# Optimization experiments

Measured on AMD Instinct MI355X. Metric: run time of the kernel, lower is better.

Reference implementation:

```python
import jax, jax.numpy as jnp
import numpy as np

VOCAB = 32000
EMBED = 512
NUM_CLASS = 5
LEAVES = 8192
N_NODES = 2 * LEAVES - 1


def _build_tree(n_leaves):
    """Balanced binary tree over n_leaves leaves, nodes listed in post-order
    (children always appear before their parent), matching the recursive
    traversal order of the original torch module."""
    is_leaf, word, left, right = [], [], [], []

    def rec(lo, hi):
        if hi - lo == 1:
            is_leaf.append(1)
            word.append((lo * 2654435761) % VOCAB)
            left.append(0)
            right.append(0)
        else:
            mid = (lo + hi) // 2
            l = rec(lo, mid)
            r = rec(mid, hi)
            is_leaf.append(0)
            word.append(0)
            left.append(l)
            right.append(r)
        return len(is_leaf) - 1

    rec(0, n_leaves)
    return (np.asarray(is_leaf, np.int32), np.asarray(word, np.int32),
            np.asarray(left, np.int32), np.asarray(right, np.int32))


def setup_inputs() -> dict:
    key = jax.random.key(0)
    k1, k2, k3, k4, k5 = jax.random.split(key, 5)
    is_leaf, word, left, right = _build_tree(LEAVES)
    scale = 0.05
    return {
        "is_leaf": jnp.asarray(is_leaf),
        "word": jnp.asarray(word),
        "left": jnp.asarray(left),
        "right": jnp.asarray(right),
        "emb": jax.random.normal(k1, (VOCAB, EMBED), jnp.float32) * scale,
        "W": jax.random.normal(k2, (EMBED, 2 * EMBED), jnp.float32) * scale,
        "bW": jax.random.normal(k3, (EMBED,), jnp.float32) * scale,
        "P": jax.random.normal(k4, (NUM_CLASS, EMBED), jnp.float32) * scale,
        "bP": jax.random.normal(k5, (NUM_CLASS,), jnp.float32) * scale,
    }


def reference(is_leaf, word, left, right, emb, W, bW, P, bP):
    n = is_leaf.shape[0]

    def step(H, xs):
        idx, lf, wd, li, ri = xs
        # internal node: relu(W @ [h_left; h_right] + b)
        pair = jnp.concatenate([H[li], H[ri]])          # [2D]
        internal = pair @ W.T + bW                       # [D]
        leaf = emb[wd]                                   # [D]
        h = jax.nn.relu(jnp.where(lf == 1, leaf, internal))
        return H.at[idx].set(h), None

    H0 = jnp.zeros((n, EMBED), emb.dtype)
    xs = (jnp.arange(n, dtype=jnp.int32), is_leaf, word, left, right)
    H, _ = jax.lax.scan(step, H0, xs)
    # per-node class logits, rows in traversal (post-)order: [N, num_class]
    return H @ P.T + bP
```

## Files before the change

### kernel.cpp

```cpp
#include <hip/hip_runtime.h>


#define EMBED 512
#define K2    1024
#define WOFF  (EMBED * K2)

typedef _Float16 half8 __attribute__((ext_vector_type(8)));
typedef float    floatx4 __attribute__((ext_vector_type(4)));

__device__ __forceinline__ float relu_f(float x) { return fmaxf(x, 0.0f); }

#define GLDS16(gp, lp)                                                        \
    __builtin_amdgcn_global_load_lds(                                         \
        (const __attribute__((address_space(1))) void*)(gp),                  \
        (__attribute__((address_space(3))) void*)(lp), 16, 0, 0)

#define MFMA16(a, b, c) __builtin_amdgcn_mfma_f32_16x16x32_f16(a, b, c, 0, 0, 0)

__global__ __launch_bounds__(256)
void packleaf(const float* __restrict__ W, const float* __restrict__ emb,
              const int* __restrict__ word,
              _Float16* __restrict__ Whp,
              _Float16* __restrict__ Hh, _Float16* __restrict__ Hl,
              int nLeaves)
{
    int tid = threadIdx.x;
    int wave = tid >> 6, lane = tid & 63;

    {
        int t = blockIdx.x * 256 + tid;
        int n = t >> 7, kc = t & 127;
        const float* src = W + (size_t)n * K2 + kc * 8;
        int s = kc >> 2, quad = kc & 3;
        int ln = (quad << 4) | (n & 15);
        size_t off = (size_t)(n >> 4) * 16384 + (size_t)s * 512 + (size_t)ln * 8;
        half8 hi, lo;
#pragma unroll
        for (int j = 0; j < 8; ++j) {
            float w = src[j];
            _Float16 h16 = (_Float16)w;
            hi[j] = h16;
            lo[j] = (_Float16)(w - (float)h16);
        }
        *(half8*)(Whp + off) = hi;
        *(half8*)(Whp + WOFF + off) = lo;
    }
    {
#pragma unroll
        for (int i = 0; i < 8; ++i) {
            int m = blockIdx.x * 32 + wave * 8 + i;
            if (m < nLeaves) {
                int wd = word[2 * m - __popc(m)];
                const float4* src = (const float4*)(emb + (size_t)wd * EMBED) + lane * 2;
                float4 a = src[0], b = src[1];
                float v[8] = {a.x, a.y, a.z, a.w, b.x, b.y, b.z, b.w};
                half8 hi, lo;
#pragma unroll
                for (int j = 0; j < 8; ++j) {
                    float x = relu_f(v[j]);
                    _Float16 h16 = (_Float16)x;
                    hi[j] = h16;
                    lo[j] = (_Float16)(x - (float)h16);
                }
                *(half8*)(Hh + (size_t)m * EMBED + lane * 8) = hi;
                *(half8*)(Hl + (size_t)m * EMBED + lane * 8) = lo;
            }
        }
    }
}

__global__ __launch_bounds__(256)
void gemm_lvl(const _Float16* __restrict__ Ap,
              const _Float16* __restrict__ Wp,
              const float* __restrict__ bW,
              _Float16* __restrict__ Cp,
              int hoff)
{
    __shared__ _Float16 As[16384];
    __shared__ float Red[4096];

    int tid = threadIdx.x;
    int wave = tid >> 6, lane = tid & 63;
    int q = lane >> 4, r = lane & 15;
    int slice = wave >> 1, nh = wave & 1;
    int bm0 = blockIdx.x * 64, bn0 = blockIdx.y * 64;

    const _Float16* Asrc = Ap + (size_t)(nh ? hoff : 0)
                         + (size_t)(bm0 + r) * 1024 + slice * 512 + q * 8;

    floatx4 acc[4][2];
#pragma unroll
    for (int t = 0; t < 4; ++t)
#pragma unroll
        for (int u = 0; u < 2; ++u) acc[t][u] = (floatx4){0.f, 0.f, 0.f, 0.f};

    for (int kc = 0; kc < 8; ++kc) {
#pragma unroll
        for (int t = 0; t < 4; ++t)
#pragma unroll
            for (int s2 = 0; s2 < 2; ++s2) {
                const _Float16* gp = Asrc + t * (16 * 1024) + kc * 64 + s2 * 32;
                GLDS16(gp, &As[(slice * 16 + t * 4 + s2 * 2 + nh) * 512]);
            }
        __syncthreads();

#pragma unroll
        for (int s2 = 0; s2 < 2; ++s2) {
            half8 bh[2], bl[2];
#pragma unroll
            for (int u = 0; u < 2; ++u) {
                const _Float16* pb = Wp + (size_t)(blockIdx.y * 4 + nh * 2 + u) * 16384
                                   + (size_t)(slice * 16 + kc * 2 + s2) * 512 + lane * 8;
                bh[u] = *(const half8*)pb;
                bl[u] = *(const half8*)(pb + WOFF);
            }
#pragma unroll
            for (int t = 0; t < 4; ++t) {
                half8 ah = *(const half8*)&As[(slice * 16 + t * 4 + s2 * 2 + 0) * 512 + lane * 8];
                half8 al = *(const half8*)&As[(slice * 16 + t * 4 + s2 * 2 + 1) * 512 + lane * 8];
#pragma unroll
                for (int u = 0; u < 2; ++u) {
                    acc[t][u] = MFMA16(ah, bh[u], acc[t][u]);
                    acc[t][u] = MFMA16(ah, bl[u], acc[t][u]);
                    acc[t][u] = MFMA16(al, bh[u], acc[t][u]);
                }
            }
        }
        __syncthreads();
    }

    if (slice == 1) {
#pragma unroll
        for (int t = 0; t < 4; ++t)
#pragma unroll
            for (int u = 0; u < 2; ++u)
#pragma unroll
                for (int reg = 0; reg < 4; ++reg)
                    Red[(t * 16 + q * 4 + reg) * 64 + nh * 32 + u * 16 + r]
                        = acc[t][u][reg];
    }
    __syncthreads();
    if (slice == 0) {
#pragma unroll
        for (int t = 0; t < 4; ++t)
#pragma unroll
            for (int u = 0; u < 2; ++u) {
                int col = bn0 + nh * 32 + u * 16 + r;
                float bw = bW[col];
#pragma unroll
                for (int reg = 0; reg < 4; ++reg) {
                    int ml = t * 16 + q * 4 + reg;
                    float v = acc[t][u][reg]
                            + Red[ml * 64 + nh * 32 + u * 16 + r];
                    float x = relu_f(v + bw);
                    _Float16 hi = (_Float16)x;
                    size_t o = (size_t)(bm0 + ml) * EMBED + col;
                    Cp[o] = hi;
                    Cp[o + hoff] = (_Float16)(x - (float)hi);
                }
            }
    }
}

__global__ __launch_bounds__(256)
void gemm_splitk32(const _Float16* __restrict__ Ap, const _Float16* __restrict__ Wp,
                   const float* __restrict__ bW,
                   _Float16* __restrict__ Cp, int hoff)
{
    __shared__ float red[4096];

    int tid = threadIdx.x;
    int wave = tid >> 6, lane = tid & 63;
    int q = lane >> 4, r = lane & 15;
    int m0 = blockIdx.x * 32, n0 = blockIdx.y * 32;

    const _Float16 *pAh[2], *pAl[2];
#pragma unroll
    for (int mi = 0; mi < 2; ++mi) {
        int m = m0 + mi * 16 + r;
        int prow = 2 * m + (wave >> 1);
        int kb = (wave & 1) * 256;
        pAh[mi] = Ap + (size_t)prow * EMBED + kb + q * 8;
        pAl[mi] = pAh[mi] + hoff;
    }
    const _Float16* pB[2];
#pragma unroll
    for (int u = 0; u < 2; ++u)
        pB[u] = Wp + (size_t)(blockIdx.y * 2 + u) * 16384
              + (size_t)(wave * 8) * 512 + lane * 8;

    floatx4 acc[2][2];
#pragma unroll
    for (int mi = 0; mi < 2; ++mi)
#pragma unroll
        for (int u = 0; u < 2; ++u) acc[mi][u] = (floatx4){0.f, 0.f, 0.f, 0.f};

#pragma unroll
    for (int s = 0; s < 8; ++s) {
        half8 ah[2], al[2], bh[2], bl[2];
#pragma unroll
        for (int mi = 0; mi < 2; ++mi) {
            ah[mi] = *(const half8*)(pAh[mi] + s * 32);
            al[mi] = *(const half8*)(pAl[mi] + s * 32);
        }
#pragma unroll
        for (int u = 0; u < 2; ++u) {
            bh[u] = *(const half8*)(pB[u] + s * 512);
            bl[u] = *(const half8*)(pB[u] + s * 512 + WOFF);
        }
#pragma unroll
        for (int mi = 0; mi < 2; ++mi)
#pragma unroll
            for (int u = 0; u < 2; ++u) {
                acc[mi][u] = MFMA16(ah[mi], bh[u], acc[mi][u]);
                acc[mi][u] = MFMA16(ah[mi], bl[u], acc[mi][u]);
                acc[mi][u] = MFMA16(al[mi], bh[u], acc[mi][u]);
            }
    }

#pragma unroll
    for (int mi = 0; mi < 2; ++mi)
#pragma unroll
        for (int u = 0; u < 2; ++u)
#pragma unroll
            for (int reg = 0; reg < 4; ++reg)
                red[wave * 1024 + (mi * 16 + q * 4 + reg) * 32 + u * 16 + r]
                    = acc[mi][u][reg];
    __syncthreads();

    int row = tid >> 3, c4 = (tid & 7) * 4;
    _Float16 hi4[4], lo4[4];
#pragma unroll
    for (int j = 0; j < 4; ++j) {
        int c = row * 32 + c4 + j;
        float v = red[c] + red[1024 + c] + red[2048 + c] + red[3072 + c];
        float x = relu_f(v + bW[n0 + c4 + j]);
        _Float16 hi = (_Float16)x;
        hi4[j] = hi;
        lo4[j] = (_Float16)(x - (float)hi);
    }
    size_t o = (size_t)(m0 + row) * EMBED + n0 + c4;
#pragma unroll
    for (int j = 0; j < 4; ++j) { Cp[o + j] = hi4[j]; Cp[o + hoff + j] = lo4[j]; }
}

__global__ __launch_bounds__(256)
void gemm_splitk(const _Float16* __restrict__ Ap, const _Float16* __restrict__ Wp,
                 const float* __restrict__ bW,
                 _Float16* __restrict__ Cp, int hoff, int M)
{
    __shared__ float red[1024];

    int tid = threadIdx.x;
    int wave = tid >> 6, lane = tid & 63;
    int q = lane >> 4, r = lane & 15;
    int mt = blockIdx.x, u = blockIdx.y;

    int m = mt * 16 + r;
    if (m >= M) m = M - 1;
    int prow = 2 * m + (wave >> 1);
    int kb = (wave & 1) * 256;
    const _Float16* pAh = Ap + (size_t)prow * EMBED + kb + q * 8;
    const _Float16* pAl = pAh + hoff;
    const _Float16* pB  = Wp + (size_t)u * 16384 + (size_t)(wave * 8) * 512 + lane * 8;

    floatx4 acc = (floatx4){0.f, 0.f, 0.f, 0.f};
#pragma unroll
    for (int s = 0; s < 8; ++s) {
        half8 ah = *(const half8*)(pAh + s * 32);
        half8 al = *(const half8*)(pAl + s * 32);
        half8 bh = *(const half8*)(pB + s * 512);
        half8 bl = *(const half8*)(pB + s * 512 + WOFF);
        acc = MFMA16(ah, bh, acc);
        acc = MFMA16(ah, bl, acc);
        acc = MFMA16(al, bh, acc);
    }
#pragma unroll
    for (int reg = 0; reg < 4; ++reg)
        red[wave * 256 + (q * 4 + reg) * 16 + r] = acc[reg];
    __syncthreads();

    int row = tid >> 4, col = tid & 15;
    float v = red[row * 16 + col] + red[256 + row * 16 + col]
            + red[512 + row * 16 + col] + red[768 + row * 16 + col];
    int mm = mt * 16 + row;
    if (mm < M) {
        int colg = u * 16 + col;
        float x = relu_f(v + bW[colg]);
        _Float16 hi = (_Float16)x;
        size_t o = (size_t)mm * EMBED + colg;
        Cp[o] = hi;
        Cp[o + hoff] = (_Float16)(x - (float)hi);
    }
}

__global__ __launch_bounds__(256)
void out_kernel(const _Float16* __restrict__ Hh, const _Float16* __restrict__ Hl,
                const float* __restrict__ P, const float* __restrict__ bP,
                float* __restrict__ out, int nNodes)
{
    int t = blockIdx.x * 256 + threadIdx.x;
    int j = t >> 6, lane = t & 63;
    if (j >= nNodes) return;
    int v = nNodes - j;
    int h = 13 - (31 - __clz(v));
    int m = j - ((nNodes + 1) - (1 << (13 - h + 1)));
    int node = ((m + 1) << (h + 1)) - 2 - __popc(m);

    half8 hv = *(const half8*)(Hh + (size_t)j * EMBED + lane * 8);
    half8 lv = *(const half8*)(Hl + (size_t)j * EMBED + lane * 8);
    float hx[8];
#pragma unroll
    for (int k = 0; k < 8; ++k) hx[k] = (float)hv[k] + (float)lv[k];
    float s[5];
#pragma unroll
    for (int c = 0; c < 5; ++c) {
        const float* p = P + c * EMBED + lane * 8;
        float4 p0 = *(const float4*)p;
        float4 p1 = *(const float4*)(p + 4);
        s[c] = hx[0] * p0.x + hx[1] * p0.y + hx[2] * p0.z + hx[3] * p0.w
             + hx[4] * p1.x + hx[5] * p1.y + hx[6] * p1.z + hx[7] * p1.w;
    }
#pragma unroll
    for (int o = 32; o > 0; o >>= 1)
#pragma unroll
        for (int c = 0; c < 5; ++c)
            s[c] += __shfl_down(s[c], o, 64);
    if (lane == 0) {
#pragma unroll
        for (int c = 0; c < 5; ++c)
            out[(size_t)node * 5 + c] = s[c] + bP[c];
    }
}

extern "C" void kernel_launch(void* const* d_in, const int* in_sizes, int n_in,
                              void* d_out, int out_size, void* d_ws, size_t ws_size,
                              hipStream_t stream)
{
    const int*   word = (const int*)d_in[1];
    const float* emb  = (const float*)d_in[4];
    const float* W    = (const float*)d_in[5];
    const float* bW   = (const float*)d_in[6];
    const float* P    = (const float*)d_in[7];
    const float* bP   = (const float*)d_in[8];
    float* out = (float*)d_out;

    int nNodes  = in_sizes[0];
    int nLeaves = (nNodes + 1) / 2;
    int nRows   = nNodes + 1;

    int hoff = nRows * EMBED;
    _Float16* Hh  = (_Float16*)d_ws;
    _Float16* Hl  = Hh + hoff;
    _Float16* Whp = Hl + hoff;

    auto roff = [&](int h) { return nRows - (1 << (14 - h)); };

    packleaf<<<dim3(256), dim3(256), 0, stream>>>(
        W, emb, word, Whp, Hh, Hl, nLeaves);

    for (int h = 1; h <= 2; ++h) {
        int M = 1 << (13 - h);
        gemm_lvl<<<dim3(M / 64, 8), dim3(256), 0, stream>>>(
            Hh + (size_t)roff(h - 1) * EMBED, Whp, bW,
            Hh + (size_t)roff(h) * EMBED, hoff);
    }
    for (int h = 3; h <= 4; ++h) {
        int M = 1 << (13 - h);
        gemm_splitk32<<<dim3(M / 32, 16), dim3(256), 0, stream>>>(
            Hh + (size_t)roff(h - 1) * EMBED, Whp, bW,
            Hh + (size_t)roff(h) * EMBED, hoff);
    }
    for (int h = 5; h <= 13; ++h) {
        int M = 1 << (13 - h);
        gemm_splitk<<<dim3((M + 15) / 16, 32), dim3(256), 0, stream>>>(
            Hh + (size_t)roff(h - 1) * EMBED, Whp, bW,
            Hh + (size_t)roff(h) * EMBED, hoff, M);
    }
    out_kernel<<<dim3((nNodes * 64 + 255) / 256), dim3(256), 0, stream>>>(
        Hh, Hl, P, bP, out, nNodes);
}
```

Measured before the change: 235.5 us.

## Replace split-K level GEMM with double-buffered full-K 128-row tiles

The first two tree-level GEMMs now use a templated kernel with 128-row tiles where each wave owns 32 rows across the full K=1024. This removes the split-K LDS reduction and the extra barrier. A/Alow tiles are double-buffered in LDS through async global-to-LDS loads with explicit vmcnt waits, so loads overlap with MFMA work. The N-tile width is templated per level (128 or 64 columns) to keep grid sizes at 128 blocks. The larger LDS footprint and fewer blocks may reduce occupancy.

Measured after the change: 290.3 us. 23.2% more time.

```diff
diff --git a/kernel.cpp b/kernel.cpp
--- a/kernel.cpp
+++ b/kernel.cpp
@@ -69,97 +69,101 @@
     }
 }
 
-__global__ __launch_bounds__(256)
-void gemm_lvl(const _Float16* __restrict__ Ap,
+template <int BNF>
+__global__ __launch_bounds__(256, 2)
+void gemm_big(const _Float16* __restrict__ Ap,
               const _Float16* __restrict__ Wp,
               const float* __restrict__ bW,
               _Float16* __restrict__ Cp,
               int hoff)
 {
-    __shared__ _Float16 As[16384];
-    __shared__ float Red[4096];
+    __shared__ _Float16 As[32768];
 
     int tid = threadIdx.x;
-    int wave = tid >> 6, lane = tid & 63;
+    int w = tid >> 6, lane = tid & 63;
     int q = lane >> 4, r = lane & 15;
-    int slice = wave >> 1, nh = wave & 1;
-    int bm0 = blockIdx.x * 64, bn0 = blockIdx.y * 64;
-
-    const _Float16* Asrc = Ap + (size_t)(nh ? hoff : 0)
-                         + (size_t)(bm0 + r) * 1024 + slice * 512 + q * 8;
-
-    floatx4 acc[4][2];
-#pragma unroll
-    for (int t = 0; t < 4; ++t)
-#pragma unroll
-        for (int u = 0; u < 2; ++u) acc[t][u] = (floatx4){0.f, 0.f, 0.f, 0.f};
-
-    for (int kc = 0; kc < 8; ++kc) {
-#pragma unroll
-        for (int t = 0; t < 4; ++t)
-#pragma unroll
-            for (int s2 = 0; s2 < 2; ++s2) {
-                const _Float16* gp = Asrc + t * (16 * 1024) + kc * 64 + s2 * 32;
-                GLDS16(gp, &As[(slice * 16 + t * 4 + s2 * 2 + nh) * 512]);
-            }
-        __syncthreads();
+    int bm0 = blockIdx.x * 128;
+    int bn0 = blockIdx.y * (BNF * 16);
+
+    const _Float16* Asrc = Ap + (size_t)(bm0 + w * 32 + r) * 1024 + q * 8;
+
+    floatx4 acc[2][BNF];
+#pragma unroll
+    for (int t2 = 0; t2 < 2; ++t2)
+#pragma unroll
+        for (int u = 0; u < BNF; ++u) acc[t2][u] = (floatx4){0.f, 0.f, 0.f, 0.f};
+
+#pragma unroll
+    for (int t2 = 0; t2 < 2; ++t2)
+#pragma unroll
+        for (int s2 = 0; s2 < 2; ++s2)
+#pragma unroll
+            for (int hl = 0; hl < 2; ++hl) {
+                const _Float16* gp = Asrc + (size_t)hl * hoff
+                                   + t2 * (16 * 1024) + s2 * 32;
+                GLDS16(gp, &As[(((w * 2 + t2) * 2 + s2) * 2 + hl) * 512]);
+            }
+
+    for (int kc = 0; kc < 16; ++kc) {
+        int buf = kc & 1;
+        if (kc < 15) {
+#pragma unroll
+            for (int t2 = 0; t2 < 2; ++t2)
+#pragma unroll
+                for (int s2 = 0; s2 < 2; ++s2)
+#pragma unroll
+                    for (int hl = 0; hl < 2; ++hl) {
+                        const _Float16* gp = Asrc + (size_t)hl * hoff
+                                           + t2 * (16 * 1024) + (kc + 1) * 64 + s2 * 32;
+                        GLDS16(gp, &As[((buf ^ 1) * 32
+                                        + ((w * 2 + t2) * 2 + s2) * 2 + hl) * 512]);
+                    }
+            asm volatile("s_waitcnt vmcnt(8)" ::: "memory");
+        } else {
+            asm volatile("s_waitcnt vmcnt(0)" ::: "memory");
+        }
 
 #pragma unroll
         for (int s2 = 0; s2 < 2; ++s2) {
-            half8 bh[2], bl[2];
-#pragma unroll
-            for (int u = 0; u < 2; ++u) {
-                const _Float16* pb = Wp + (size_t)(blockIdx.y * 4 + nh * 2 + u) * 16384
-                                   + (size_t)(slice * 16 + kc * 2 + s2) * 512 + lane * 8;
-                bh[u] = *(const half8*)pb;
-                bl[u] = *(const half8*)(pb + WOFF);
-            }
-#pragma unroll
-            for (int t = 0; t < 4; ++t) {
-                half8 ah = *(const half8*)&As[(slice * 16 + t * 4 + s2 * 2 + 0) * 512 + lane * 8];
-                half8 al = *(const half8*)&As[(slice * 16 + t * 4 + s2 * 2 + 1) * 512 + lane * 8];
-#pragma unroll
-                for (int u = 0; u < 2; ++u) {
-                    acc[t][u] = MFMA16(ah, bh[u], acc[t][u]);
-                    acc[t][u] = MFMA16(ah, bl[u], acc[t][u]);
-                    acc[t][u] = MFMA16(al, bh[u], acc[t][u]);
+            half8 ah[2], al[2];
+#pragma unroll
+            for (int t2 = 0; t2 < 2; ++t2) {
+                int slot = buf * 32 + ((w * 2 + t2) * 2 + s2) * 2;
+                ah[t2] = *(const half8*)&As[slot * 512 + lane * 8];
+                al[t2] = *(const half8*)&As[(slot + 1) * 512 + lane * 8];
+            }
+#pragma unroll
+            for (int u = 0; u < BNF; ++u) {
+                const _Float16* pb = Wp + (size_t)(blockIdx.y * BNF + u) * 16384
+                                   + (size_t)(kc * 2 + s2) * 512 + lane * 8;
+                half8 bh = *(const half8*)pb;
+                half8 bl = *(const half8*)(pb + WOFF);
+#pragma unroll
+                for (int t2 = 0; t2 < 2; ++t2) {
+                    acc[t2][u] = MFMA16(ah[t2], bh, acc[t2][u]);
+                    acc[t2][u] = MFMA16(ah[t2], bl, acc[t2][u]);
+                    acc[t2][u] = MFMA16(al[t2], bh, acc[t2][u]);
                 }
             }
         }
-        __syncthreads();
-    }
-
-    if (slice == 1) {
-#pragma unroll
-        for (int t = 0; t < 4; ++t)
-#pragma unroll
-            for (int u = 0; u < 2; ++u)
-#pragma unroll
-                for (int reg = 0; reg < 4; ++reg)
-                    Red[(t * 16 + q * 4 + reg) * 64 + nh * 32 + u * 16 + r]
-                        = acc[t][u][reg];
-    }
-    __syncthreads();
-    if (slice == 0) {
-#pragma unroll
-        for (int t = 0; t < 4; ++t)
-#pragma unroll
-            for (int u = 0; u < 2; ++u) {
-                int col = bn0 + nh * 32 + u * 16 + r;
-                float bw = bW[col];
-#pragma unroll
-                for (int reg = 0; reg < 4; ++reg) {
-                    int ml = t * 16 + q * 4 + reg;
-                    float v = acc[t][u][reg]
-                            + Red[ml * 64 + nh * 32 + u * 16 + r];
-                    float x = relu_f(v + bw);
-                    _Float16 hi = (_Float16)x;
-                    size_t o = (size_t)(bm0 + ml) * EMBED + col;
-                    Cp[o] = hi;
-                    Cp[o + hoff] = (_Float16)(x - (float)hi);
-                }
-            }
-    }
+    }
+
+#pragma unroll
+    for (int t2 = 0; t2 < 2; ++t2)
+#pragma unroll
+        for (int u = 0; u < BNF; ++u) {
+            int col = bn0 + u * 16 + r;
+            float bw = bW[col];
+#pragma unroll
+            for (int reg = 0; reg < 4; ++reg) {
+                int row = bm0 + (w * 2 + t2) * 16 + q * 4 + reg;
+                float x = relu_f(acc[t2][u][reg] + bw);
+                _Float16 hi = (_Float16)x;
+                size_t o = (size_t)row * EMBED + col;
+                Cp[o] = hi;
+                Cp[o + hoff] = (_Float16)(x - (float)hi);
+            }
+        }
 }
 
 __global__ __launch_bounds__(256)
@@ -359,12 +363,13 @@
     packleaf<<<dim3(256), dim3(256), 0, stream>>>(
         W, emb, word, Whp, Hh, Hl, nLeaves);
 
-    for (int h = 1; h <= 2; ++h) {
-        int M = 1 << (13 - h);
-        gemm_lvl<<<dim3(M / 64, 8), dim3(256), 0, stream>>>(
-            Hh + (size_t)roff(h - 1) * EMBED, Whp, bW,
-            Hh + (size_t)roff(h) * EMBED, hoff);
-    }
+    gemm_big<8><<<dim3(32, 4), dim3(256), 0, stream>>>(
+        Hh + (size_t)roff(0) * EMBED, Whp, bW,
+        Hh + (size_t)roff(1) * EMBED, hoff);
+    gemm_big<4><<<dim3(16, 8), dim3(256), 0, stream>>>(
+        Hh + (size_t)roff(1) * EMBED, Whp, bW,
+        Hh + (size_t)roff(2) * EMBED, hoff);
+
     for (int h = 3; h <= 4; ++h) {
         int M = 1 << (13 - h);
         gemm_splitk32<<<dim3(M / 32, 16), dim3(256), 0, stream>>>(
```

## Fuse class-logit projection into leaf and level GEMM epilogues via atomics

Applied to the files above, without the earlier changes.

Removes the separate output kernel that reread all hidden states to compute per-node logits. Each leaf-packing block and each level GEMM epilogue now computes partial dot products of its fresh activations with P and atomically accumulates them into outputs pre-initialised with bP by a new init kernel. This avoids a full pass over the hi/lo hidden buffers. In exchange it adds an extra launch, extra syncs and shared-memory traffic in gemm_lvl, float atomics whose summation order is nondeterministic, and logits computed from fp32 values instead of the hi+lo reconstruction.

New measurement: 274.7 us. 16.6% more time.

```diff
diff --git a/kernel.cpp b/kernel.cpp
--- a/kernel.cpp
+++ b/kernel.cpp
@@ -16,13 +16,21 @@
         (__attribute__((address_space(3))) void*)(lp), 16, 0, 0)
 
 #define MFMA16(a, b, c) __builtin_amdgcn_mfma_f32_16x16x32_f16(a, b, c, 0, 0, 0)
+
+__global__ __launch_bounds__(256)
+void init_out(const float* __restrict__ bP, float* __restrict__ out, int n5)
+{
+    int i = blockIdx.x * 256 + threadIdx.x;
+    if (i < n5) out[i] = bP[i - (i / 5) * 5];
+}
 
 __global__ __launch_bounds__(256)
 void packleaf(const float* __restrict__ W, const float* __restrict__ emb,
               const int* __restrict__ word,
               _Float16* __restrict__ Whp,
               _Float16* __restrict__ Hh, _Float16* __restrict__ Hl,
-              int nLeaves)
+              const float* __restrict__ P, const float* __restrict__ bP,
+              float* __restrict__ out, int nLeaves)
 {
     int tid = threadIdx.x;
     int wave = tid >> 6, lane = tid & 63;
@@ -50,20 +58,42 @@
         for (int i = 0; i < 8; ++i) {
             int m = blockIdx.x * 32 + wave * 8 + i;
             if (m < nLeaves) {
-                int wd = word[2 * m - __popc(m)];
+                int node = 2 * m - __popc(m);
+                int wd = word[node];
                 const float4* src = (const float4*)(emb + (size_t)wd * EMBED) + lane * 2;
                 float4 a = src[0], b = src[1];
                 float v[8] = {a.x, a.y, a.z, a.w, b.x, b.y, b.z, b.w};
+                float xs[8];
                 half8 hi, lo;
 #pragma unroll
                 for (int j = 0; j < 8; ++j) {
                     float x = relu_f(v[j]);
+                    xs[j] = x;
                     _Float16 h16 = (_Float16)x;
                     hi[j] = h16;
                     lo[j] = (_Float16)(x - (float)h16);
                 }
                 *(half8*)(Hh + (size_t)m * EMBED + lane * 8) = hi;
                 *(half8*)(Hl + (size_t)m * EMBED + lane * 8) = lo;
+                float s[5];
+#pragma unroll
+                for (int c = 0; c < 5; ++c) {
+                    const float* p = P + c * EMBED + lane * 8;
+                    float4 p0 = *(const float4*)p;
+                    float4 p1 = *(const float4*)(p + 4);
+                    s[c] = xs[0] * p0.x + xs[1] * p0.y + xs[2] * p0.z + xs[3] * p0.w
+                         + xs[4] * p1.x + xs[5] * p1.y + xs[6] * p1.z + xs[7] * p1.w;
+                }
+#pragma unroll
+                for (int o = 32; o > 0; o >>= 1)
+#pragma unroll
+                    for (int c = 0; c < 5; ++c)
+                        s[c] += __shfl_down(s[c], o, 64);
+                if (lane == 0) {
+#pragma unroll
+                    for (int c = 0; c < 5; ++c)
+                        out[(size_t)node * 5 + c] = s[c] + bP[c];
+                }
             }
         }
     }
@@ -74,7 +104,8 @@
               const _Float16* __restrict__ Wp,
               const float* __restrict__ bW,
               _Float16* __restrict__ Cp,
-              int hoff)
+              int hoff,
+              const float* __restrict__ P, float* __restrict__ out, int lvl)
 {
     __shared__ _Float16 As[16384];
     __shared__ float Red[4096];
@@ -129,6 +160,7 @@
         __syncthreads();
     }
 
+    float xv[4][2][4];
     if (slice == 1) {
 #pragma unroll
         for (int t = 0; t < 4; ++t)
@@ -153,6 +185,7 @@
                     float v = acc[t][u][reg]
                             + Red[ml * 64 + nh * 32 + u * 16 + r];
                     float x = relu_f(v + bw);
+                    xv[t][u][reg] = x;
                     _Float16 hi = (_Float16)x;
                     size_t o = (size_t)(bm0 + ml) * EMBED + col;
                     Cp[o] = hi;
@@ -160,12 +193,50 @@
                 }
             }
     }
+    __syncthreads();
+    if (slice == 0) {
+#pragma unroll
+        for (int t = 0; t < 4; ++t)
+#pragma unroll
+            for (int u = 0; u < 2; ++u)
+#pragma unroll
+            for (int reg = 0; reg < 4; ++reg)
+                Red[(t * 16 + q * 4 + reg) * 64 + nh * 32 + u * 16 + r]
+                    = xv[t][u][reg];
+    }
+    __syncthreads();
+    {
+        int prow = tid >> 2, seg = tid & 3;
+        float s[5] = {0.f, 0.f, 0.f, 0.f, 0.f};
+#pragma unroll
+        for (int j4 = 0; j4 < 4; ++j4) {
+            floatx4 xq = *(const floatx4*)&Red[prow * 64 + seg * 16 + j4 * 4];
+#pragma unroll
+            for (int c = 0; c < 5; ++c) {
+                float4 pq = *(const float4*)&P[c * EMBED + bn0 + seg * 16 + j4 * 4];
+                s[c] += xq[0] * pq.x + xq[1] * pq.y + xq[2] * pq.z + xq[3] * pq.w;
+            }
+        }
+#pragma unroll
+        for (int c = 0; c < 5; ++c) {
+            s[c] += __shfl_xor(s[c], 1, 64);
+            s[c] += __shfl_xor(s[c], 2, 64);
+        }
+        if (seg == 0) {
+            int mrow = bm0 + prow;
+            int node = ((mrow + 1) << (lvl + 1)) - 2 - __popc(mrow);
+#pragma unroll
+            for (int c = 0; c < 5; ++c)
+                atomicAdd(&out[(size_t)node * 5 + c], s[c]);
+        }
+    }
 }
 
 __global__ __launch_bounds__(256)
 void gemm_splitk32(const _Float16* __restrict__ Ap, const _Float16* __restrict__ Wp,
                    const float* __restrict__ bW,
-                   _Float16* __restrict__ Cp, int hoff)
+                   _Float16* __restrict__ Cp, int hoff,
+                   const float* __restrict__ P, float* __restrict__ out, int lvl)
 {
     __shared__ float red[4096];
 
@@ -229,12 +300,14 @@
     __syncthreads();
 
     int row = tid >> 3, c4 = (tid & 7) * 4;
+    float xf[4];
     _Float16 hi4[4], lo4[4];
 #pragma unroll
     for (int j = 0; j < 4; ++j) {
         int c = row * 32 + c4 + j;
         float v = red[c] + red[1024 + c] + red[2048 + c] + red[3072 + c];
         float x = relu_f(v + bW[n0 + c4 + j]);
+        xf[j] = x;
         _Float16 hi = (_Float16)x;
         hi4[j] = hi;
         lo4[j] = (_Float16)(x - (float)hi);
@@ -242,12 +315,32 @@
     size_t o = (size_t)(m0 + row) * EMBED + n0 + c4;
 #pragma unroll
     for (int j = 0; j < 4; ++j) { Cp[o + j] = hi4[j]; Cp[o + hoff + j] = lo4[j]; }
+
+    {
+        float s[5];
+#pragma unroll
+        for (int c = 0; c < 5; ++c) {
+            float4 pq = *(const float4*)&P[c * EMBED + n0 + c4];
+            s[c] = xf[0] * pq.x + xf[1] * pq.y + xf[2] * pq.z + xf[3] * pq.w;
+            s[c] += __shfl_xor(s[c], 1, 64);
+            s[c] += __shfl_xor(s[c], 2, 64);
+            s[c] += __shfl_xor(s[c], 4, 64);
+        }
+        if ((tid & 7) == 0) {
+            int mrow = m0 + row;
+            int node = ((mrow + 1) << (lvl + 1)) - 2 - __popc(mrow);
+#pragma unroll
+            for (int c = 0; c < 5; ++c)
+                atomicAdd(&out[(size_t)node * 5 + c], s[c]);
+        }
+    }
 }
 
 __global__ __launch_bounds__(256)
 void gemm_splitk(const _Float16* __restrict__ Ap, const _Float16* __restrict__ Wp,
                  const float* __restrict__ bW,
-                 _Float16* __restrict__ Cp, int hoff, int M)
+                 _Float16* __restrict__ Cp, int hoff, int M,
+                 const float* __restrict__ P, float* __restrict__ out, int lvl)
 {
     __shared__ float red[1024];
 
@@ -284,52 +377,30 @@
     float v = red[row * 16 + col] + red[256 + row * 16 + col]
             + red[512 + row * 16 + col] + red[768 + row * 16 + col];
     int mm = mt * 16 + row;
+    int colg = u * 16 + col;
+    float x = relu_f(v + bW[colg]);
     if (mm < M) {
-        int colg = u * 16 + col;
-        float x = relu_f(v + bW[colg]);
         _Float16 hi = (_Float16)x;
         size_t o = (size_t)mm * EMBED + colg;
         Cp[o] = hi;
         Cp[o + hoff] = (_Float16)(x - (float)hi);
     }
-}
-
-__global__ __launch_bounds__(256)
-void out_kernel(const _Float16* __restrict__ Hh, const _Float16* __restrict__ Hl,
-                const float* __restrict__ P, const float* __restrict__ bP,
-                float* __restrict__ out, int nNodes)
-{
-    int t = blockIdx.x * 256 + threadIdx.x;
-    int j = t >> 6, lane = t & 63;
-    if (j >= nNodes) return;
-    int v = nNodes - j;
-    int h = 13 - (31 - __clz(v));
-    int m = j - ((nNodes + 1) - (1 << (13 - h + 1)));
-    int node = ((m + 1) << (h + 1)) - 2 - __popc(m);
-
-    half8 hv = *(const half8*)(Hh + (size_t)j * EMBED + lane * 8);
-    half8 lv = *(const half8*)(Hl + (size_t)j * EMBED + lane * 8);
-    float hx[8];
-#pragma unroll
-    for (int k = 0; k < 8; ++k) hx[k] = (float)hv[k] + (float)lv[k];
-    float s[5];
-#pragma unroll
-    for (int c = 0; c < 5; ++c) {
-        const float* p = P + c * EMBED + lane * 8;
-        float4 p0 = *(const float4*)p;
-        float4 p1 = *(const float4*)(p + 4);
-        s[c] = hx[0] * p0.x + hx[1] * p0.y + hx[2] * p0.z + hx[3] * p0.w
-             + hx[4] * p1.x + hx[5] * p1.y + hx[6] * p1.z + hx[7] * p1.w;
-    }
-#pragma unroll
-    for (int o = 32; o > 0; o >>= 1)
-#pragma unroll
-        for (int c = 0; c < 5; ++c)
-            s[c] += __shfl_down(s[c], o, 64);
-    if (lane == 0) {
-#pragma unroll
-        for (int c = 0; c < 5; ++c)
-            out[(size_t)node * 5 + c] = s[c] + bP[c];
+    {
+        float s[5];
+#pragma unroll
+        for (int c = 0; c < 5; ++c) {
+            s[c] = x * P[c * EMBED + colg];
+            s[c] += __shfl_xor(s[c], 1, 64);
+            s[c] += __shfl_xor(s[c], 2, 64);
+            s[c] += __shfl_xor(s[c], 4, 64);
+            s[c] += __shfl_xor(s[c], 8, 64);
+        }
+        if (col == 0 && mm < M) {
+            int node = ((mm + 1) << (lvl + 1)) - 2 - __popc(mm);
+#pragma unroll
+            for (int c = 0; c < 5; ++c)
+                atomicAdd(&out[(size_t)node * 5 + c], s[c]);
+        }
     }
 }
 
@@ -356,27 +427,28 @@
 
     auto roff = [&](int h) { return nRows - (1 << (14 - h)); };
 
+    int n5 = nNodes * 5;
+    init_out<<<dim3((n5 + 255) / 256), dim3(256), 0, stream>>>(bP, out, n5);
+
     packleaf<<<dim3(256), dim3(256), 0, stream>>>(
-        W, emb, word, Whp, Hh, Hl, nLeaves);
+        W, emb, word, Whp, Hh, Hl, P, bP, out, nLeaves);
 
     for (int h = 1; h <= 2; ++h) {
         int M = 1 << (13 - h);
         gemm_lvl<<<dim3(M / 64, 8), dim3(256), 0, stream>>>(
             Hh + (size_t)roff(h - 1) * EMBED, Whp, bW,
-            Hh + (size_t)roff(h) * EMBED, hoff);
+            Hh + (size_t)roff(h) * EMBED, hoff, P, out, h);
     }
     for (int h = 3; h <= 4; ++h) {
         int M = 1 << (13 - h);
         gemm_splitk32<<<dim3(M / 32, 16), dim3(256), 0, stream>>>(
             Hh + (size_t)roff(h - 1) * EMBED, Whp, bW,
-            Hh + (size_t)roff(h) * EMBED, hoff);
+            Hh + (size_t)roff(h) * EMBED, hoff, P, out, h);
     }
     for (int h = 5; h <= 13; ++h) {
         int M = 1 << (13 - h);
         gemm_splitk<<<dim3((M + 15) / 16, 32), dim3(256), 0, stream>>>(
             Hh + (size_t)roff(h - 1) * EMBED, Whp, bW,
-            Hh + (size_t)roff(h) * EMBED, hoff, M);
-    }
-    out_kernel<<<dim3((nNodes * 64 + 255) / 256), dim3(256), 0, stream>>>(
-        Hh, Hl, P, bP, out, nNodes);
-}
+            Hh + (size_t)roff(h) * EMBED, hoff, M, P, out, h);
+    }
+}
```
